# Kernel tuning notes

Hardware: AMD Instinct MI355X
Metric: run time of the kernel (lower is better)

Reference implementation:

```python
import jax, jax.numpy as jnp
import numpy as np

N, E = 20000, 640000
ND, ED = 16, 8            # raw node/edge feature dims
H = 128                   # encoder hidden = gnn channels = mlp hidden
OUT = 2
L = 10                    # gnn layers (shared weights, per-layer layernorms)
NOISE_STD = 0.003
EPS = 1e-5


def _mlp(x, w1, b1, w2, b2):
    return jax.nn.relu(x @ w1 + b1) @ w2 + b2


def _ln(x, g, b):
    m = jnp.mean(x, axis=-1, keepdims=True)
    v = jnp.var(x, axis=-1, keepdims=True)
    return (x - m) * jax.lax.rsqrt(v + EPS) * g + b


def setup_inputs() -> dict:
    key = jax.random.key(0)
    ks = jax.random.split(key, 32)

    def w(k, i, o):
        return jax.random.normal(k, (i, o), jnp.float32) / np.sqrt(i)

    inp = {
        "x": jax.random.normal(ks[0], (N, ND), jnp.float32),
        "edge_attr": jax.random.normal(ks[1], (E, ED), jnp.float32),
        "edge_index": jax.random.randint(ks[2], (2, E), 0, N, jnp.int64),
        "node_noise": jax.random.normal(ks[3], (N, ND), jnp.float32) * NOISE_STD,
        "edge_noise": jax.random.normal(ks[4], (E, ED), jnp.float32) * NOISE_STD,
        # encoders
        "node_enc_w1": w(ks[5], ND, H), "node_enc_b1": jnp.zeros((H,), jnp.float32),
        "node_enc_w2": w(ks[6], H, H),  "node_enc_b2": jnp.zeros((H,), jnp.float32),
        "edge_enc_w1": w(ks[7], ED, H), "edge_enc_b1": jnp.zeros((H,), jnp.float32),
        "edge_enc_w2": w(ks[8], H, H),  "edge_enc_b2": jnp.zeros((H,), jnp.float32),
        # single shared MPNN (module instance reused across all L layers)
        "gnn_edge_w1": w(ks[9], 3 * H, H), "gnn_edge_b1": jnp.zeros((H,), jnp.float32),
        "gnn_edge_w2": w(ks[10], H, H),    "gnn_edge_b2": jnp.zeros((H,), jnp.float32),
        "gnn_node_w1": w(ks[11], 2 * H, H), "gnn_node_b1": jnp.zeros((H,), jnp.float32),
        "gnn_node_w2": w(ks[12], H, H),     "gnn_node_b2": jnp.zeros((H,), jnp.float32),
        # per-layer layernorms
        "x_ln_g": jnp.ones((L, H), jnp.float32), "x_ln_b": jnp.zeros((L, H), jnp.float32),
        "e_ln_g": jnp.ones((L, H), jnp.float32), "e_ln_b": jnp.zeros((L, H), jnp.float32),
        # decoder
        "dec_w1": w(ks[13], H, H),  "dec_b1": jnp.zeros((H,), jnp.float32),
        "dec_w2": w(ks[14], H, OUT), "dec_b2": jnp.zeros((OUT,), jnp.float32),
    }
    return inp


def reference(x, edge_attr, edge_index, node_noise, edge_noise,
              node_enc_w1, node_enc_b1, node_enc_w2, node_enc_b2,
              edge_enc_w1, edge_enc_b1, edge_enc_w2, edge_enc_b2,
              gnn_edge_w1, gnn_edge_b1, gnn_edge_w2, gnn_edge_b2,
              gnn_node_w1, gnn_node_b1, gnn_node_w2, gnn_node_b2,
              x_ln_g, x_ln_b, e_ln_g, e_ln_b,
              dec_w1, dec_b1, dec_w2, dec_b2):
    src = edge_index[0]  # x_j
    dst = edge_index[1]  # x_i (aggregation target)

    h = _mlp(x + node_noise, node_enc_w1, node_enc_b1, node_enc_w2, node_enc_b2)      # [N,H]
    e = _mlp(edge_attr + edge_noise, edge_enc_w1, edge_enc_b1, edge_enc_w2, edge_enc_b2)  # [E,H]

    for l in range(L):
        xi = h[dst]  # [E,H]
        xj = h[src]  # [E,H]
        # edge update: e + edge_mlp([x_i, x_j, e])
        e_new = e + _mlp(jnp.concatenate([xi, xj, e], axis=1),
                         gnn_edge_w1, gnn_edge_b1, gnn_edge_w2, gnn_edge_b2)
        # message: x_i + node_mlp([x_i, e_new]); aggr='add' over dst
        msg = xi + _mlp(jnp.concatenate([xi, e_new], axis=1),
                        gnn_node_w1, gnn_node_b1, gnn_node_w2, gnn_node_b2)
        h_agg = jax.ops.segment_sum(msg, dst, num_segments=N)
        h = _ln(h + h_agg, x_ln_g[l], x_ln_b[l])
        e = _ln(e + e_new, e_ln_g[l], e_ln_b[l])

    out = _mlp(h, dec_w1, dec_b1, dec_w2, dec_b2) - node_noise[:, :OUT]
    return out
```

## Files before the change

kernel.cpp:

```cpp
#include <hip/hip_runtime.h>
#include <stdio.h>

#define NN 20000
#define NE 640000
#define NL 10

typedef unsigned short u16;
typedef unsigned int u32;
typedef __attribute__((ext_vector_type(8))) __bf16 bf16x8;
typedef __attribute__((ext_vector_type(8))) unsigned short us8;
typedef __attribute__((ext_vector_type(4))) float f32x4;

__device__ __forceinline__ bf16x8 ldbf(const u16* p) {
  union { us8 u; bf16x8 b; } v;
  v.u = *(const us8*)p;
  return v.b;
}
__device__ __forceinline__ f32x4 zero4() {
  f32x4 z; z[0] = 0.f; z[1] = 0.f; z[2] = 0.f; z[3] = 0.f; return z;
}
__device__ __forceinline__ float bf2f(u16 u) {
  u32 x = ((u32)u) << 16;
  return __uint_as_float(x);
}
__device__ __forceinline__ u16 f2bf(float f) {
  u32 x = __float_as_uint(f);
  u32 r = (x + 0x7fffu + ((x >> 16) & 1u)) >> 16;
  return (u16)r;
}
__device__ __forceinline__ int lad(int row, int col) {
  return (row << 7) + ((((col >> 3) ^ (row & 15)) << 3) | (col & 7));
}
__device__ __forceinline__ uint2 pack4bf(const float f[4]) {
  uint2 u;
  u.x = (u32)f2bf(f[0]) | ((u32)f2bf(f[1]) << 16);
  u.y = (u32)f2bf(f[2]) | ((u32)f2bf(f[3]) << 16);
  return u;
}
__device__ __forceinline__ void unpack4bf(uint2 u, float f[4]) {
  f[0] = bf2f((u16)(u.x & 0xffffu)); f[1] = bf2f((u16)(u.x >> 16));
  f[2] = bf2f((u16)(u.y & 0xffffu)); f[3] = bf2f((u16)(u.y >> 16));
}

__global__ void LearnedSimModel_28716151341396_kernel() {}

__global__ void init_kernel(float* agg, int agg_n, int* cnt, int cnt_n) {
  int i = blockIdx.x * 256 + threadIdx.x;
  if (i < agg_n) agg[i] = 0.0f;
  if (i < cnt_n) cnt[i] = 0;
}

__global__ void idx_detect_kernel(const int* raw, int* flag) {
  if (threadIdx.x == 0 && blockIdx.x == 0) {
    int any = 0;
    for (int k = 0; k < 16; ++k) any = any | raw[2 * k + 1];
    flag[0] = (any != 0) ? 1 : 0;
  }
}

__global__ void idx_prep_kernel(const int* raw, const int* flag, int* idx0) {
  int i = blockIdx.x * 256 + threadIdx.x;
  if (i < 2 * NE) {
    int v;
    if (flag[0] != 0) v = raw[i];
    else v = (int)(((const long long*)raw)[i]);
    if (v < 0) v = 0;
    if (v >= NN) v = NN - 1;
    idx0[i] = v;
  }
}

__global__ void hist_kernel(const int* dst0, int* cnt) {
  int i = blockIdx.x * 256 + threadIdx.x;
  if (i < NE) atomicAdd(&cnt[dst0[i]], 1);
}

__global__ void prefix_kernel(const int* cnt, int* cursor) {
  __shared__ int buf[1024];
  __shared__ int carry;
  int t = threadIdx.x;
  if (t == 0) carry = 0;
  __syncthreads();
  for (int base = 0; base < NN; base += 1024) {
    int v = (base + t < NN) ? cnt[base + t] : 0;
    buf[t] = v;
    __syncthreads();
    for (int s = 1; s < 1024; s <<= 1) {
      int add = (t >= s) ? buf[t - s] : 0;
      __syncthreads();
      buf[t] += add;
      __syncthreads();
    }
    int excl = buf[t] - v + carry;
    if (base + t < NN) cursor[base + t] = excl;
    __syncthreads();
    if (t == 0) carry = carry + buf[1023];
    __syncthreads();
  }
}

__global__ void scatter_kernel(const int* src0, const int* dst0, int* cursor,
                               int* src_s, int* dst_s, int* perm) {
  int i = blockIdx.x * 256 + threadIdx.x;
  if (i < NE) {
    int d = dst0[i];
    int pos = atomicAdd(&cursor[d], 1);
    perm[pos] = i;
    src_s[pos] = src0[i];
    dst_s[pos] = d;
  }
}

__global__ void transpose_slice_kernel(const float* __restrict__ W,
                                       u16* __restrict__ Wt, int koff) {
  int i = blockIdx.x * 256 + threadIdx.x;
  int k = i >> 7, f = i & 127;
  Wt[f * 128 + k] = f2bf(W[(size_t)(koff + k) * 128 + f]);
}

__global__ void node_enc_kernel(const float* x, const float* noise,
                                const float* w1, const float* b1,
                                const float* w2, const float* b2,
                                float* h, u16* h16) {
  __shared__ float in16[16];
  __shared__ float t1s[128];
  int f = threadIdx.x;
  int n = blockIdx.x;
  if (f < 16) in16[f] = x[n * 16 + f] + noise[n * 16 + f];
  __syncthreads();
  float a = b1[f];
  for (int k = 0; k < 16; ++k) a += in16[k] * w1[k * 128 + f];
  t1s[f] = fmaxf(a, 0.0f);
  __syncthreads();
  float o = b2[f];
  for (int k = 0; k < 128; ++k) o += t1s[k] * w2[k * 128 + f];
  h[(long long)n * 128 + f] = o;
  h16[(long long)n * 128 + f] = f2bf(o);
}

__device__ __forceinline__ void gemm128(const u16* lds, const u16* Wt,
                                        int l16, int quad, int fb, f32x4 acc[2][4]) {
  for (int ks = 0; ks < 4; ++ks) {
    int kg = ks * 32 + quad * 8;
    bf16x8 b0 = ldbf(lds + lad(0 * 16 + l16, kg));
    bf16x8 b1 = ldbf(lds + lad(1 * 16 + l16, kg));
    bf16x8 b2 = ldbf(lds + lad(2 * 16 + l16, kg));
    bf16x8 b3 = ldbf(lds + lad(3 * 16 + l16, kg));
    for (int tt = 0; tt < 2; ++tt) {
      bf16x8 a = ldbf(Wt + (size_t)(fb + tt * 16 + l16) * 128 + kg);
      acc[tt][0] = __builtin_amdgcn_mfma_f32_16x16x32_bf16(a, b0, acc[tt][0], 0, 0, 0);
      acc[tt][1] = __builtin_amdgcn_mfma_f32_16x16x32_bf16(a, b1, acc[tt][1], 0, 0, 0);
      acc[tt][2] = __builtin_amdgcn_mfma_f32_16x16x32_bf16(a, b2, acc[tt][2], 0, 0, 0);
      acc[tt][3] = __builtin_amdgcn_mfma_f32_16x16x32_bf16(a, b3, acc[tt][3], 0, 0, 0);
    }
  }
}

__global__ __launch_bounds__(256) void edge_enc_mfma(
    const float* __restrict__ attr, const float* __restrict__ noise,
    const int* __restrict__ perm,
    const float* __restrict__ w1, const float* __restrict__ b1,
    const u16* __restrict__ Wt2, const float* __restrict__ b2,
    u16* __restrict__ e)
{
  __shared__ __align__(16) u16 sT[64 * 128];
  __shared__ float sIn[64][8];
  __shared__ int sPerm[64];

  const int t = threadIdx.x;
  if (t < 64) sPerm[t] = perm[blockIdx.x * 64 + t];
  __syncthreads();

  for (int it = 0; it < 2; ++it) {
    int c = t + it * 256;
    int row = c >> 3, k = c & 7;
    int p = sPerm[row];
    sIn[row][k] = attr[(size_t)p * 8 + k] + noise[(size_t)p * 8 + k];
  }
  __syncthreads();

  {
    int f = t & 127;
    int r0 = (t >> 7) * 32;
    float wc[8];
    for (int k = 0; k < 8; ++k) wc[k] = w1[k * 128 + f];
    float bb = b1[f];
    for (int j = 0; j < 32; ++j) {
      int row = r0 + j;
      float a = bb;
      for (int k = 0; k < 8; ++k) a += sIn[row][k] * wc[k];
      sT[lad(row, f)] = f2bf(fmaxf(a, 0.f));
    }
  }
  __syncthreads();

  const int lane = t & 63;
  const int wave = t >> 6;
  const int l16 = lane & 15;
  const int quad = lane >> 4;
  const int fb = wave * 32;
  f32x4 acc[2][4];
  for (int tt = 0; tt < 2; ++tt)
    for (int et = 0; et < 4; ++et) acc[tt][et] = zero4();
  gemm128(sT, Wt2, l16, quad, fb, acc);
  u16* etile = e + (size_t)blockIdx.x * 8192;
  for (int tt = 0; tt < 2; ++tt) {
    int f0 = fb + tt * 16 + quad * 4;
    float4 bb = *(const float4*)(b2 + f0);
    float bbv[4] = {bb.x, bb.y, bb.z, bb.w};
    for (int et = 0; et < 4; ++et) {
      int row = et * 16 + l16;
      float o[4];
      for (int r = 0; r < 4; ++r) o[r] = acc[tt][et][r] + bbv[r];
      *(uint2*)(etile + lad(row, f0)) = pack4bf(o);
    }
  }
}

__global__ __launch_bounds__(256) void nprep_kernel(
    const u16* __restrict__ h16, const u16* __restrict__ Wt_np,
    float* __restrict__ nprep)
{
  __shared__ __align__(16) u16 sH[64 * 128];
  const int t = threadIdx.x;
  const int n0 = blockIdx.x * 64;

  for (int it = 0; it < 4; ++it) {
    int c = t + it * 256;
    int row = c >> 4, seg = c & 15;
    int n = n0 + row;
    if (n >= NN) n = NN - 1;
    us8 v = *(const us8*)(h16 + (size_t)n * 128 + seg * 8);
    *(us8*)(sH + ((row << 7) + ((seg ^ (row & 15)) << 3))) = v;
  }
  __syncthreads();

  const int lane = t & 63;
  const int wave = t >> 6;
  const int l16 = lane & 15;
  const int quad = lane >> 4;
  const int fb = wave * 96;
  f32x4 acc[6][4];
  for (int ft = 0; ft < 6; ++ft)
    for (int et = 0; et < 4; ++et) acc[ft][et] = zero4();
  for (int ks = 0; ks < 4; ++ks) {
    int kg = ks * 32 + quad * 8;
    bf16x8 b0 = ldbf(sH + lad(0 * 16 + l16, kg));
    bf16x8 b1 = ldbf(sH + lad(1 * 16 + l16, kg));
    bf16x8 b2 = ldbf(sH + lad(2 * 16 + l16, kg));
    bf16x8 b3 = ldbf(sH + lad(3 * 16 + l16, kg));
    for (int ft = 0; ft < 6; ++ft) {
      bf16x8 a = ldbf(Wt_np + (size_t)(fb + ft * 16 + l16) * 128 + kg);
      acc[ft][0] = __builtin_amdgcn_mfma_f32_16x16x32_bf16(a, b0, acc[ft][0], 0, 0, 0);
      acc[ft][1] = __builtin_amdgcn_mfma_f32_16x16x32_bf16(a, b1, acc[ft][1], 0, 0, 0);
      acc[ft][2] = __builtin_amdgcn_mfma_f32_16x16x32_bf16(a, b2, acc[ft][2], 0, 0, 0);
      acc[ft][3] = __builtin_amdgcn_mfma_f32_16x16x32_bf16(a, b3, acc[ft][3], 0, 0, 0);
    }
  }
  for (int ft = 0; ft < 6; ++ft) {
    int f0 = fb + ft * 16 + quad * 4;
    for (int et = 0; et < 4; ++et) {
      int n = n0 + et * 16 + l16;
      if (n < NN) *(f32x4*)(nprep + (size_t)n * 384 + f0) = acc[ft][et];
    }
  }
}

__global__ __launch_bounds__(256, 4) void gnn_edge_mfma(
    u16* __restrict__ eg,
    const int* __restrict__ src_s, const int* __restrict__ dst_s,
    const float* __restrict__ nprep,
    const u16* __restrict__ Wt_e1c, const float* __restrict__ be1,
    const u16* __restrict__ Wt_e2,  const float* __restrict__ be2,
    const u16* __restrict__ Wt_n1b, const float* __restrict__ bn1,
    const u16* __restrict__ Wt_n2,
    const float* __restrict__ lng, const float* __restrict__ lnb,
    float* __restrict__ agg)
{
  __shared__ __align__(16) char smem[35328];
  u16* sE = (u16*)smem;
  u16* sT = (u16*)(smem + 16384);
  float* msgf = (float*)smem;
  float* part_s = (float*)(smem + 32768);
  float* part_q = (float*)(smem + 33792);
  int* sDst = (int*)(smem + 34816);
  int* sSrc = (int*)(smem + 35072);

  const int t = threadIdx.x;
  const int e0 = blockIdx.x * 64;
  const int lane = t & 63;
  const int wave = t >> 6;
  const int l16 = lane & 15;
  const int quad = lane >> 4;
  const int fb = wave * 32;

  if (t < 64) { sDst[t] = dst_s[e0 + t]; sSrc[t] = src_s[e0 + t]; }

  const u16* ebase = eg + (size_t)blockIdx.x * 8192;
  for (int it = 0; it < 4; ++it) {
    int c = it * 2048 + t * 8;
    *(us8*)(sE + c) = *(const us8*)(ebase + c);
  }
  __syncthreads();

  int rd[4], rs[4];
  for (int et = 0; et < 4; ++et) {
    rd[et] = sDst[et * 16 + l16];
    rs[et] = sSrc[et * 16 + l16];
  }

  f32x4 acc[2][4];
  for (int tt = 0; tt < 2; ++tt)
    for (int et = 0; et < 4; ++et) acc[tt][et] = zero4();
  gemm128(sE, Wt_e1c, l16, quad, fb, acc);
  for (int tt = 0; tt < 2; ++tt) {
    int f0 = fb + tt * 16 + quad * 4;
    float4 bb = *(const float4*)(be1 + f0);
    float bbv[4] = {bb.x, bb.y, bb.z, bb.w};
    f32x4 av[4], jv[4];
    for (int et = 0; et < 4; ++et) {
      av[et] = *(const f32x4*)(nprep + (size_t)rd[et] * 384 + f0);
      jv[et] = *(const f32x4*)(nprep + (size_t)rs[et] * 384 + 128 + f0);
    }
    for (int et = 0; et < 4; ++et) {
      int row = et * 16 + l16;
      float o[4];
      for (int r = 0; r < 4; ++r)
        o[r] = fmaxf(acc[tt][et][r] + av[et][r] + jv[et][r] + bbv[r], 0.f);
      *(uint2*)(sT + lad(row, f0)) = pack4bf(o);
    }
  }
  __syncthreads();

  for (int tt = 0; tt < 2; ++tt)
    for (int et = 0; et < 4; ++et) acc[tt][et] = zero4();
  gemm128(sT, Wt_e2, l16, quad, fb, acc);
  float lnv[2][4][4];
  for (int tt = 0; tt < 2; ++tt) {
    int f0 = fb + tt * 16 + quad * 4;
    float4 bb = *(const float4*)(be2 + f0);
    float bbv[4] = {bb.x, bb.y, bb.z, bb.w};
    for (int et = 0; et < 4; ++et) {
      int row = et * 16 + l16;
      float eo[4];
      unpack4bf(*(const uint2*)(sE + lad(row, f0)), eo);
      float en[4];
      for (int r = 0; r < 4; ++r) {
        en[r] = eo[r] + acc[tt][et][r] + bbv[r];
        lnv[tt][et][r] = eo[r] + en[r];
      }
      *(uint2*)(sE + lad(row, f0)) = pack4bf(en);
    }
  }
  for (int et = 0; et < 4; ++et) {
    float s = 0.f, q = 0.f;
    for (int tt = 0; tt < 2; ++tt)
      for (int r = 0; r < 4; ++r) {
        float v = lnv[tt][et][r];
        s += v; q += v * v;
      }
    s += __shfl_xor(s, 16); s += __shfl_xor(s, 32);
    q += __shfl_xor(q, 16); q += __shfl_xor(q, 32);
    if (quad == 0) {
      part_s[wave * 64 + et * 16 + l16] = s;
      part_q[wave * 64 + et * 16 + l16] = q;
    }
  }
  __syncthreads();

  u16* etile = eg + (size_t)blockIdx.x * 8192;
  for (int et = 0; et < 4; ++et) {
    int row = et * 16 + l16;
    float s = part_s[row] + part_s[64 + row] + part_s[128 + row] + part_s[192 + row];
    float q = part_q[row] + part_q[64 + row] + part_q[128 + row] + part_q[192 + row];
    float m = s * (1.f / 128.f);
    float var = q * (1.f / 128.f) - m * m;
    float rsv = rsqrtf(fmaxf(var, 0.f) + 1e-5f);
    for (int tt = 0; tt < 2; ++tt) {
      int f0 = fb + tt * 16 + quad * 4;
      float4 g4 = *(const float4*)(lng + f0);
      float4 b4 = *(const float4*)(lnb + f0);
      float gv[4] = {g4.x, g4.y, g4.z, g4.w};
      float bv[4] = {b4.x, b4.y, b4.z, b4.w};
      float o[4];
      for (int r = 0; r < 4; ++r)
        o[r] = (lnv[tt][et][r] - m) * rsv * gv[r] + bv[r];
      *(uint2*)(etile + lad(row, f0)) = pack4bf(o);
    }
  }

  for (int tt = 0; tt < 2; ++tt)
    for (int et = 0; et < 4; ++et) acc[tt][et] = zero4();
  gemm128(sE, Wt_n1b, l16, quad, fb, acc);
  for (int tt = 0; tt < 2; ++tt) {
    int f0 = fb + tt * 16 + quad * 4;
    float4 bb = *(const float4*)(bn1 + f0);
    float bbv[4] = {bb.x, bb.y, bb.z, bb.w};
    f32x4 bv4[4];
    for (int et = 0; et < 4; ++et)
      bv4[et] = *(const f32x4*)(nprep + (size_t)rd[et] * 384 + 256 + f0);
    for (int et = 0; et < 4; ++et) {
      int row = et * 16 + l16;
      float o[4];
      for (int r = 0; r < 4; ++r)
        o[r] = fmaxf(acc[tt][et][r] + bv4[et][r] + bbv[r], 0.f);
      *(uint2*)(sT + lad(row, f0)) = pack4bf(o);
    }
  }
  __syncthreads();

  for (int tt = 0; tt < 2; ++tt)
    for (int et = 0; et < 4; ++et) acc[tt][et] = zero4();
  gemm128(sT, Wt_n2, l16, quad, fb, acc);
  __syncthreads();

  for (int tt = 0; tt < 2; ++tt) {
    int f0 = fb + tt * 16 + quad * 4;
    for (int et = 0; et < 4; ++et) {
      int row = et * 16 + l16;
      *(f32x4*)(msgf + row * 128 + (((f0 >> 2) ^ (row & 31)) << 2)) = acc[tt][et];
    }
  }
  __syncthreads();

  {
    int f = t & 127, half = t >> 7;
    int j0 = half * 32;
    int c = f >> 2, c3 = f & 3;
    float a = 0.f;
    for (int j = j0; j < j0 + 32; ++j) {
      a += msgf[j * 128 + ((c ^ (j & 31)) << 2) + c3];
      int dj = sDst[j];
      if (j == j0 + 31 || sDst[j + 1] != dj) {
        atomicAdd(&agg[(size_t)dj * 128 + f], a);
        a = 0.f;
      }
    }
  }
}

__global__ void node_ln_kernel(float* h, u16* h16, float* agg,
                               const int* cnt, const float* bn2,
                               const float* g, const float* b) {
  __shared__ float red[128];
  int f = threadIdx.x;
  int n = blockIdx.x;
  long long base = (long long)n * 128 + f;
  float deg = (float)cnt[n];
  float hv = h[base];
  float v = hv + agg[base] + deg * (hv + bn2[f]);
  red[f] = v;
  __syncthreads();
  for (int s = 64; s > 0; s >>= 1) {
    if (f < s) red[f] += red[f + s];
    __syncthreads();
  }
  float m = red[0] * (1.0f / 128.0f);
  __syncthreads();
  red[f] = v * v;
  __syncthreads();
  for (int s = 64; s > 0; s >>= 1) {
    if (f < s) red[f] += red[f + s];
    __syncthreads();
  }
  float q = red[0] * (1.0f / 128.0f);
  float var = q - m * m;
  float rs = rsqrtf(fmaxf(var, 0.0f) + 1e-5f);
  float o = (v - m) * rs * g[f] + b[f];
  h[base] = o;
  h16[base] = f2bf(o);
  agg[base] = 0.0f;
}

__global__ void decoder_kernel(const float* h, const float* w1, const float* b1,
                               const float* w2, const float* b2,
                               const float* noise, float* out) {
  __shared__ float t1s[128];
  int f = threadIdx.x;
  int n = blockIdx.x;
  float a = b1[f];
  for (int k = 0; k < 128; ++k) a += h[(long long)n * 128 + k] * w1[k * 128 + f];
  t1s[f] = fmaxf(a, 0.0f);
  __syncthreads();
  if (f < 2) {
    float s = b2[f];
    for (int k = 0; k < 128; ++k) s += t1s[k] * w2[k * 2 + f];
    s -= noise[n * 16 + f];
    out[n * 2 + f] = s;
  }
}

extern "C" void kernel_launch(void* const* d_in, const int* in_sizes, int n_in,
                              void* d_out, int out_size, void* d_ws, size_t ws_size,
                              hipStream_t stream) {
  (void)in_sizes; (void)n_in; (void)out_size; (void)ws_size;

  const float* x      = (const float*)d_in[0];
  const float* eattr  = (const float*)d_in[1];
  const int*   eidx   = (const int*)d_in[2];
  const float* nnoise = (const float*)d_in[3];
  const float* enoise = (const float*)d_in[4];
  const float* ne_w1 = (const float*)d_in[5];  const float* ne_b1 = (const float*)d_in[6];
  const float* ne_w2 = (const float*)d_in[7];  const float* ne_b2 = (const float*)d_in[8];
  const float* ee_w1 = (const float*)d_in[9];  const float* ee_b1 = (const float*)d_in[10];
  const float* ee_w2 = (const float*)d_in[11]; const float* ee_b2 = (const float*)d_in[12];
  const float* ge_w1 = (const float*)d_in[13]; const float* ge_b1 = (const float*)d_in[14];
  const float* ge_w2 = (const float*)d_in[15]; const float* ge_b2 = (const float*)d_in[16];
  const float* gn_w1 = (const float*)d_in[17]; const float* gn_b1 = (const float*)d_in[18];
  const float* gn_w2 = (const float*)d_in[19]; const float* gn_b2 = (const float*)d_in[20];
  const float* xlng = (const float*)d_in[21]; const float* xlnb = (const float*)d_in[22];
  const float* elng = (const float*)d_in[23]; const float* elnb = (const float*)d_in[24];
  const float* d_w1 = (const float*)d_in[25]; const float* d_b1 = (const float*)d_in[26];
  const float* d_w2 = (const float*)d_in[27]; const float* d_b2 = (const float*)d_in[28];

  float* out = (float*)d_out;

  char* base = (char*)d_ws;
  size_t off = 0;
  int* idx0 = (int*)(base + off);    off += (size_t)2 * NE * 4;
  int* src_s = (int*)(base + off);   off += (size_t)NE * 4;
  int* dst_s = (int*)(base + off);   off += (size_t)NE * 4;
  int* perm = (int*)(base + off);    off += (size_t)NE * 4;
  int* cnt = (int*)(base + off);     off += (size_t)NN * 4;
  int* cursor = (int*)(base + off);  off += (size_t)NN * 4;
  int* flag = (int*)(base + off);    off += 16;
  float* h = (float*)(base + off);   off += (size_t)NN * 128 * 4;
  u16* h16 = (u16*)(base + off);     off += (size_t)NN * 128 * 2;
  float* agg = (float*)(base + off); off += (size_t)NN * 128 * 4;
  u16* e = (u16*)(base + off);       off += (size_t)NE * 128 * 2;
  float* nprep = (float*)(base + off); off += (size_t)NN * 384 * 4;
  u16* Wt_np = (u16*)(base + off);   off += (size_t)384 * 128 * 2;
  u16* Wt_e1c = (u16*)(base + off);  off += (size_t)128 * 128 * 2;
  u16* Wt_ge2 = (u16*)(base + off);  off += (size_t)128 * 128 * 2;
  u16* Wt_n1b = (u16*)(base + off);  off += (size_t)128 * 128 * 2;
  u16* Wt_gn2 = (u16*)(base + off);  off += (size_t)128 * 128 * 2;
  u16* Wt_ee2 = (u16*)(base + off);  off += (size_t)128 * 128 * 2;

  hipStreamCaptureStatus cs = hipStreamCaptureStatusNone;
  hipStreamIsCapturing(stream, &cs);
  const bool dbg = (cs == hipStreamCaptureStatusNone);

  const int* src0 = idx0;
  const int* dst0 = idx0 + NE;

  init_kernel<<<(NN * 128 + 255) / 256, 256, 0, stream>>>(agg, NN * 128, cnt, NN);
  idx_detect_kernel<<<1, 64, 0, stream>>>(eidx, flag);
  idx_prep_kernel<<<(2 * NE + 255) / 256, 256, 0, stream>>>(eidx, flag, idx0);

  hist_kernel<<<(NE + 255) / 256, 256, 0, stream>>>(dst0, cnt);
  prefix_kernel<<<1, 1024, 0, stream>>>(cnt, cursor);
  scatter_kernel<<<(NE + 255) / 256, 256, 0, stream>>>(src0, dst0, cursor,
                                                       src_s, dst_s, perm);

  transpose_slice_kernel<<<64, 256, 0, stream>>>(ge_w1, Wt_np, 0);
  transpose_slice_kernel<<<64, 256, 0, stream>>>(ge_w1, Wt_np + 16384, 128);
  transpose_slice_kernel<<<64, 256, 0, stream>>>(gn_w1, Wt_np + 32768, 0);
  transpose_slice_kernel<<<64, 256, 0, stream>>>(ge_w1, Wt_e1c, 256);
  transpose_slice_kernel<<<64, 256, 0, stream>>>(ge_w2, Wt_ge2, 0);
  transpose_slice_kernel<<<64, 256, 0, stream>>>(gn_w1, Wt_n1b, 128);
  transpose_slice_kernel<<<64, 256, 0, stream>>>(gn_w2, Wt_gn2, 0);
  transpose_slice_kernel<<<64, 256, 0, stream>>>(ee_w2, Wt_ee2, 0);

  node_enc_kernel<<<NN, 128, 0, stream>>>(x, nnoise, ne_w1, ne_b1, ne_w2, ne_b2, h, h16);
  edge_enc_mfma<<<NE / 64, 256, 0, stream>>>(eattr, enoise, perm,
                                             ee_w1, ee_b1, Wt_ee2, ee_b2, e);

  for (int l = 0; l < NL; ++l) {
    nprep_kernel<<<(NN + 63) / 64, 256, 0, stream>>>(h16, Wt_np, nprep);
    gnn_edge_mfma<<<NE / 64, 256, 0, stream>>>(e, src_s, dst_s, nprep,
        Wt_e1c, ge_b1, Wt_ge2, ge_b2, Wt_n1b, gn_b1, Wt_gn2,
        elng + l * 128, elnb + l * 128, agg);
    node_ln_kernel<<<NN, 128, 0, stream>>>(h, h16, agg, cnt, gn_b2,
                                           xlng + l * 128, xlnb + l * 128);
  }

  decoder_kernel<<<NN, 128, 0, stream>>>(h, d_w1, d_b1, d_w2, d_b2, nnoise, out);

  if (dbg) {
    hipStreamSynchronize(stream);
    float tbuf[6] = {0, 0, 0, 0, 0, 0};
    hipMemcpy(tbuf, h, 16, hipMemcpyDeviceToHost);
    hipMemcpy(tbuf + 4, out, 8, hipMemcpyDeviceToHost);
    fprintf(stderr, "KL r24 nprep-K128: h[0..3]=%.5g %.5g %.5g %.5g out[0..1]=%.5g %.5g lasterr=%d\n",
            tbuf[0], tbuf[1], tbuf[2], tbuf[3], tbuf[4], tbuf[5], (int)hipGetLastError());
    fflush(stderr);
  }
}
```

Baseline: 3.584 ms.

## Fuse node layernorm with projection prep, store src projection in bf16, raise occupancy

Merges the per-layer node layernorm with the node projection GEMM into one kernel, so the h16 round trip and one launch per layer go away. The gathered source-side projection is stored as bf16 (aj16) instead of fp32, halving the bytes of that random gather, while the dst-side parts stay fp32 in a 256-wide buffer. The edge kernel shrinks shared memory to 32 KB by aliasing buffers and splitting the message scatter into two halves, which allows launch_bounds 5 blocks per CU. In exchange it adds extra barriers and costs some precision on the xj term.

After: 3.900 ms. +8.8%, slower.

```diff
diff --git a/kernel.cpp b/kernel.cpp
--- a/kernel.cpp
+++ b/kernel.cpp
@@ -121,7 +121,7 @@
 __global__ void node_enc_kernel(const float* x, const float* noise,
                                 const float* w1, const float* b1,
                                 const float* w2, const float* b2,
-                                float* h, u16* h16) {
+                                float* h) {
   __shared__ float in16[16];
   __shared__ float t1s[128];
   int f = threadIdx.x;
@@ -135,7 +135,6 @@
   float o = b2[f];
   for (int k = 0; k < 128; ++k) o += t1s[k] * w2[k * 128 + f];
   h[(long long)n * 128 + f] = o;
-  h16[(long long)n * 128 + f] = f2bf(o);
 }
 
 __device__ __forceinline__ void gemm128(const u16* lds, const u16* Wt,
@@ -217,23 +216,67 @@
   }
 }
 
-__global__ __launch_bounds__(256) void nprep_kernel(
-    const u16* __restrict__ h16, const u16* __restrict__ Wt_np,
-    float* __restrict__ nprep)
+__global__ __launch_bounds__(256) void node_ln_prep(
+    float* __restrict__ h, float* __restrict__ agg,
+    const int* __restrict__ cnt, const float* __restrict__ bn2,
+    const float* __restrict__ g, const float* __restrict__ b,
+    const u16* __restrict__ Wt_np,
+    float* __restrict__ aib, u16* __restrict__ aj16, int mode)
 {
   __shared__ __align__(16) u16 sH[64 * 128];
   const int t = threadIdx.x;
   const int n0 = blockIdx.x * 64;
-
-  for (int it = 0; it < 4; ++it) {
-    int c = t + it * 256;
-    int row = c >> 4, seg = c & 15;
-    int n = n0 + row;
-    if (n >= NN) n = NN - 1;
-    us8 v = *(const us8*)(h16 + (size_t)n * 128 + seg * 8);
-    *(us8*)(sH + ((row << 7) + ((seg ^ (row & 15)) << 3))) = v;
-  }
-  __syncthreads();
+  const int row = t >> 2;
+  const int c0 = (t & 3) * 32;
+  int n = n0 + row;
+  const bool valid = n < NN;
+  const int nc = valid ? n : (NN - 1);
+
+  float v[32];
+  float* hp = h + (size_t)nc * 128 + c0;
+  if (mode & 1) {
+    float* ap = agg + (size_t)nc * 128 + c0;
+    float deg = (float)cnt[nc];
+    for (int k = 0; k < 32; k += 4) {
+      f32x4 hv = *(const f32x4*)(hp + k);
+      f32x4 av = *(const f32x4*)(ap + k);
+      f32x4 bb = *(const f32x4*)(bn2 + c0 + k);
+      for (int r = 0; r < 4; ++r) v[k + r] = hv[r] + av[r] + deg * (hv[r] + bb[r]);
+    }
+    float s = 0.f, q = 0.f;
+    for (int k = 0; k < 32; ++k) { s += v[k]; q += v[k] * v[k]; }
+    s += __shfl_xor(s, 1); s += __shfl_xor(s, 2);
+    q += __shfl_xor(q, 1); q += __shfl_xor(q, 2);
+    float m = s * (1.f / 128.f);
+    float var = q * (1.f / 128.f) - m * m;
+    float rs = rsqrtf(fmaxf(var, 0.f) + 1e-5f);
+    for (int k = 0; k < 32; k += 4) {
+      f32x4 g4 = *(const f32x4*)(g + c0 + k);
+      f32x4 b4 = *(const f32x4*)(b + c0 + k);
+      for (int r = 0; r < 4; ++r) v[k + r] = (v[k + r] - m) * rs * g4[r] + b4[r];
+    }
+    if (valid) {
+      for (int k = 0; k < 32; k += 4) {
+        f32x4 ov; for (int r = 0; r < 4; ++r) ov[r] = v[k + r];
+        *(f32x4*)(hp + k) = ov;
+        f32x4 z = zero4();
+        *(f32x4*)(ap + k) = z;
+      }
+    }
+  } else {
+    for (int k = 0; k < 32; k += 4) {
+      f32x4 hv = *(const f32x4*)(hp + k);
+      for (int r = 0; r < 4; ++r) v[k + r] = hv[r];
+    }
+  }
+  for (int k = 0; k < 32; k += 8) {
+    u16 tmp[8];
+    for (int r = 0; r < 8; ++r) tmp[r] = f2bf(v[k + r]);
+    *(uint4*)(sH + lad(row, c0 + k)) = *(const uint4*)tmp;
+  }
+  __syncthreads();
+
+  if (!(mode & 2)) return;
 
   const int lane = t & 63;
   const int wave = t >> 6;
@@ -258,18 +301,27 @@
     }
   }
   for (int ft = 0; ft < 6; ++ft) {
-    int f0 = fb + ft * 16 + quad * 4;
+    int F = fb + ft * 16 + quad * 4;
     for (int et = 0; et < 4; ++et) {
-      int n = n0 + et * 16 + l16;
-      if (n < NN) *(f32x4*)(nprep + (size_t)n * 384 + f0) = acc[ft][et];
-    }
-  }
-}
-
-__global__ __launch_bounds__(256, 4) void gnn_edge_mfma(
+      int n2 = n0 + et * 16 + l16;
+      if (n2 >= NN) continue;
+      if (F < 128) {
+        *(f32x4*)(aib + (size_t)n2 * 256 + F) = acc[ft][et];
+      } else if (F < 256) {
+        float o[4] = {acc[ft][et][0], acc[ft][et][1], acc[ft][et][2], acc[ft][et][3]};
+        *(uint2*)(aj16 + (size_t)n2 * 128 + (F - 128)) = pack4bf(o);
+      } else {
+        *(f32x4*)(aib + (size_t)n2 * 256 + (F - 128)) = acc[ft][et];
+      }
+    }
+  }
+}
+
+__global__ __launch_bounds__(256, 5) void gnn_edge_mfma(
     u16* __restrict__ eg,
     const int* __restrict__ src_s, const int* __restrict__ dst_s,
-    const float* __restrict__ nprep,
+    const float* __restrict__ aib,
+    const u16* __restrict__ aj16,
     const u16* __restrict__ Wt_e1c, const float* __restrict__ be1,
     const u16* __restrict__ Wt_e2,  const float* __restrict__ be2,
     const u16* __restrict__ Wt_n1b, const float* __restrict__ bn1,
@@ -277,14 +329,13 @@
     const float* __restrict__ lng, const float* __restrict__ lnb,
     float* __restrict__ agg)
 {
-  __shared__ __align__(16) char smem[35328];
+  __shared__ __align__(16) char smem[32768];
   u16* sE = (u16*)smem;
   u16* sT = (u16*)(smem + 16384);
+  float* part_s = (float*)(smem + 16384);
+  float* part_q = (float*)(smem + 16384 + 1024);
   float* msgf = (float*)smem;
-  float* part_s = (float*)(smem + 32768);
-  float* part_q = (float*)(smem + 33792);
-  int* sDst = (int*)(smem + 34816);
-  int* sSrc = (int*)(smem + 35072);
+  int* sDstO = (int*)(smem + 16384);
 
   const int t = threadIdx.x;
   const int e0 = blockIdx.x * 64;
@@ -294,20 +345,25 @@
   const int quad = lane >> 4;
   const int fb = wave * 32;
 
-  if (t < 64) { sDst[t] = dst_s[e0 + t]; sSrc[t] = src_s[e0 + t]; }
+  int rd[4], rs[4];
+  for (int et = 0; et < 4; ++et) {
+    rd[et] = dst_s[e0 + et * 16 + l16];
+    rs[et] = src_s[e0 + et * 16 + l16];
+  }
 
   const u16* ebase = eg + (size_t)blockIdx.x * 8192;
   for (int it = 0; it < 4; ++it) {
     int c = it * 2048 + t * 8;
     *(us8*)(sE + c) = *(const us8*)(ebase + c);
   }
-  __syncthreads();
-
-  int rd[4], rs[4];
-  for (int et = 0; et < 4; ++et) {
-    rd[et] = sDst[et * 16 + l16];
-    rs[et] = sSrc[et * 16 + l16];
-  }
+
+  uint2 jraw[2][4];
+  for (int tt = 0; tt < 2; ++tt) {
+    int f0 = fb + tt * 16 + quad * 4;
+    for (int et = 0; et < 4; ++et)
+      jraw[tt][et] = *(const uint2*)(aj16 + (size_t)rs[et] * 128 + f0);
+  }
+  __syncthreads();
 
   f32x4 acc[2][4];
   for (int tt = 0; tt < 2; ++tt)
@@ -317,16 +373,14 @@
     int f0 = fb + tt * 16 + quad * 4;
     float4 bb = *(const float4*)(be1 + f0);
     float bbv[4] = {bb.x, bb.y, bb.z, bb.w};
-    f32x4 av[4], jv[4];
     for (int et = 0; et < 4; ++et) {
-      av[et] = *(const f32x4*)(nprep + (size_t)rd[et] * 384 + f0);
-      jv[et] = *(const f32x4*)(nprep + (size_t)rs[et] * 384 + 128 + f0);
-    }
-    for (int et = 0; et < 4; ++et) {
+      f32x4 av = *(const f32x4*)(aib + (size_t)rd[et] * 256 + f0);
+      float jf[4];
+      unpack4bf(jraw[tt][et], jf);
       int row = et * 16 + l16;
       float o[4];
       for (int r = 0; r < 4; ++r)
-        o[r] = fmaxf(acc[tt][et][r] + av[et][r] + jv[et][r] + bbv[r], 0.f);
+        o[r] = fmaxf(acc[tt][et][r] + av[r] + jf[r] + bbv[r], 0.f);
       *(uint2*)(sT + lad(row, f0)) = pack4bf(o);
     }
   }
@@ -335,6 +389,7 @@
   for (int tt = 0; tt < 2; ++tt)
     for (int et = 0; et < 4; ++et) acc[tt][et] = zero4();
   gemm128(sT, Wt_e2, l16, quad, fb, acc);
+  __syncthreads();
   float lnv[2][4][4];
   for (int tt = 0; tt < 2; ++tt) {
     int f0 = fb + tt * 16 + quad * 4;
@@ -388,6 +443,7 @@
       *(uint2*)(etile + lad(row, f0)) = pack4bf(o);
     }
   }
+  __syncthreads();
 
   for (int tt = 0; tt < 2; ++tt)
     for (int et = 0; et < 4; ++et) acc[tt][et] = zero4();
@@ -396,14 +452,12 @@
     int f0 = fb + tt * 16 + quad * 4;
     float4 bb = *(const float4*)(bn1 + f0);
     float bbv[4] = {bb.x, bb.y, bb.z, bb.w};
-    f32x4 bv4[4];
-    for (int et = 0; et < 4; ++et)
-      bv4[et] = *(const f32x4*)(nprep + (size_t)rd[et] * 384 + 256 + f0);
     for (int et = 0; et < 4; ++et) {
+      f32x4 bv4 = *(const f32x4*)(aib + (size_t)rd[et] * 256 + 128 + f0);
       int row = et * 16 + l16;
       float o[4];
       for (int r = 0; r < 4; ++r)
-        o[r] = fmaxf(acc[tt][et][r] + bv4[et][r] + bbv[r], 0.f);
+        o[r] = fmaxf(acc[tt][et][r] + bv4[r] + bbv[r], 0.f);
       *(uint2*)(sT + lad(row, f0)) = pack4bf(o);
     }
   }
@@ -414,62 +468,36 @@
   gemm128(sT, Wt_n2, l16, quad, fb, acc);
   __syncthreads();
 
-  for (int tt = 0; tt < 2; ++tt) {
-    int f0 = fb + tt * 16 + quad * 4;
-    for (int et = 0; et < 4; ++et) {
-      int row = et * 16 + l16;
-      *(f32x4*)(msgf + row * 128 + (((f0 >> 2) ^ (row & 31)) << 2)) = acc[tt][et];
-    }
-  }
-  __syncthreads();
-
-  {
-    int f = t & 127, half = t >> 7;
-    int j0 = half * 32;
-    int c = f >> 2, c3 = f & 3;
-    float a = 0.f;
-    for (int j = j0; j < j0 + 32; ++j) {
-      a += msgf[j * 128 + ((c ^ (j & 31)) << 2) + c3];
-      int dj = sDst[j];
-      if (j == j0 + 31 || sDst[j + 1] != dj) {
-        atomicAdd(&agg[(size_t)dj * 128 + f], a);
-        a = 0.f;
+  if (t < 64) sDstO[t] = dst_s[e0 + t];
+
+  for (int bt = 0; bt < 2; ++bt) {
+    for (int tt = 0; tt < 2; ++tt) {
+      int f0 = fb + tt * 16 + quad * 4;
+      for (int eo2 = 0; eo2 < 2; ++eo2) {
+        int et = bt * 2 + eo2;
+        int lr = et * 16 + l16 - bt * 32;
+        *(f32x4*)(msgf + lr * 128 + ((((f0 >> 2) ^ lr) & 31) << 2)) = acc[tt][et];
       }
     }
-  }
-}
-
-__global__ void node_ln_kernel(float* h, u16* h16, float* agg,
-                               const int* cnt, const float* bn2,
-                               const float* g, const float* b) {
-  __shared__ float red[128];
-  int f = threadIdx.x;
-  int n = blockIdx.x;
-  long long base = (long long)n * 128 + f;
-  float deg = (float)cnt[n];
-  float hv = h[base];
-  float v = hv + agg[base] + deg * (hv + bn2[f]);
-  red[f] = v;
-  __syncthreads();
-  for (int s = 64; s > 0; s >>= 1) {
-    if (f < s) red[f] += red[f + s];
     __syncthreads();
-  }
-  float m = red[0] * (1.0f / 128.0f);
-  __syncthreads();
-  red[f] = v * v;
-  __syncthreads();
-  for (int s = 64; s > 0; s >>= 1) {
-    if (f < s) red[f] += red[f + s];
-    __syncthreads();
-  }
-  float q = red[0] * (1.0f / 128.0f);
-  float var = q - m * m;
-  float rs = rsqrtf(fmaxf(var, 0.0f) + 1e-5f);
-  float o = (v - m) * rs * g[f] + b[f];
-  h[base] = o;
-  h16[base] = f2bf(o);
-  agg[base] = 0.0f;
+    {
+      int f = t & 127, sub = t >> 7;
+      int c = f >> 2, c3 = f & 3;
+      float a = 0.f;
+      int jbase = bt * 32 + sub * 16;
+      for (int i = 0; i < 16; ++i) {
+        int j = jbase + i;
+        int lr = j - bt * 32;
+        a += msgf[lr * 128 + (((c ^ lr) & 31) << 2) + c3];
+        int dj = sDstO[j];
+        if (i == 15 || sDstO[j + 1] != dj) {
+          atomicAdd(&agg[(size_t)dj * 128 + f], a);
+          a = 0.f;
+        }
+      }
+    }
+    if (bt == 0) __syncthreads();
+  }
 }
 
 __global__ void decoder_kernel(const float* h, const float* w1, const float* b1,
@@ -525,10 +553,10 @@
   int* cursor = (int*)(base + off);  off += (size_t)NN * 4;
   int* flag = (int*)(base + off);    off += 16;
   float* h = (float*)(base + off);   off += (size_t)NN * 128 * 4;
-  u16* h16 = (u16*)(base + off);     off += (size_t)NN * 128 * 2;
   float* agg = (float*)(base + off); off += (size_t)NN * 128 * 4;
   u16* e = (u16*)(base + off);       off += (size_t)NE * 128 * 2;
-  float* nprep = (float*)(base + off); off += (size_t)NN * 384 * 4;
+  float* aib = (float*)(base + off); off += (size_t)NN * 256 * 4;
+  u16* aj16 = (u16*)(base + off);    off += (size_t)NN * 128 * 2;
   u16* Wt_np = (u16*)(base + off);   off += (size_t)384 * 128 * 2;
   u16* Wt_e1c = (u16*)(base + off);  off += (size_t)128 * 128 * 2;
   u16* Wt_ge2 = (u16*)(base + off);  off += (size_t)128 * 128 * 2;
@@ -561,17 +589,21 @@
   transpose_slice_kernel<<<64, 256, 0, stream>>>(gn_w2, Wt_gn2, 0);
   transpose_slice_kernel<<<64, 256, 0, stream>>>(ee_w2, Wt_ee2, 0);
 
-  node_enc_kernel<<<NN, 128, 0, stream>>>(x, nnoise, ne_w1, ne_b1, ne_w2, ne_b2, h, h16);
+  node_enc_kernel<<<NN, 128, 0, stream>>>(x, nnoise, ne_w1, ne_b1, ne_w2, ne_b2, h);
   edge_enc_mfma<<<NE / 64, 256, 0, stream>>>(eattr, enoise, perm,
                                              ee_w1, ee_b1, Wt_ee2, ee_b2, e);
 
+  const int NB_N = (NN + 63) / 64;
+  node_ln_prep<<<NB_N, 256, 0, stream>>>(h, agg, cnt, gn_b2, xlng, xlnb,
+                                         Wt_np, aib, aj16, 2);
+
   for (int l = 0; l < NL; ++l) {
-    nprep_kernel<<<(NN + 63) / 64, 256, 0, stream>>>(h16, Wt_np, nprep);
-    gnn_edge_mfma<<<NE / 64, 256, 0, stream>>>(e, src_s, dst_s, nprep,
+    gnn_edge_mfma<<<NE / 64, 256, 0, stream>>>(e, src_s, dst_s, aib, aj16,
         Wt_e1c, ge_b1, Wt_ge2, ge_b2, Wt_n1b, gn_b1, Wt_gn2,
         elng + l * 128, elnb + l * 128, agg);
-    node_ln_kernel<<<NN, 128, 0, stream>>>(h, h16, agg, cnt, gn_b2,
-                                           xlng + l * 128, xlnb + l * 128);
+    node_ln_prep<<<NB_N, 256, 0, stream>>>(h, agg, cnt, gn_b2,
+        xlng + l * 128, xlnb + l * 128, Wt_np, aib, aj16,
+        (l == NL - 1) ? 1 : 3);
   }
 
   decoder_kernel<<<NN, 128, 0, stream>>>(h, d_w1, d_b1, d_w2, d_b2, nnoise, out);
@@ -581,7 +613,7 @@
     float tbuf[6] = {0, 0, 0, 0, 0, 0};
     hipMemcpy(tbuf, h, 16, hipMemcpyDeviceToHost);
     hipMemcpy(tbuf + 4, out, 8, hipMemcpyDeviceToHost);
-    fprintf(stderr, "KL r24 nprep-K128: h[0..3]=%.5g %.5g %.5g %.5g out[0..1]=%.5g %.5g lasterr=%d\n",
+    fprintf(stderr, "KL r25 aj16-occ5: h[0..3]=%.5g %.5g %.5g %.5g out[0..1]=%.5g %.5g lasterr=%d\n",
             tbuf[0], tbuf[1], tbuf[2], tbuf[3], tbuf[4], tbuf[5], (int)hipGetLastError());
     fflush(stderr);
   }
```
